# Performance work log

Hardware: AMD Instinct MI355X
Metric: run time of the kernel (lower is better)

The kernel has to match this reference:

```python
import jax, jax.numpy as jnp
import numpy as np
from jax import lax
from jax.scipy.stats import norm

K = 2            # top-k
NUM_EXPERTS = 4
NOISE_EPS = 0.01
LOSS_COEF = 0.01


def conv3x3(x, w):
    # x: [B,Cin,H,W], w: [Cout,Cin,3,3] -> [B,Cout,H,W]
    return lax.conv_general_dilated(x, w, (1, 1), 'SAME',
                                    dimension_numbers=('NCHW', 'OIHW', 'NCHW'))


def setup_inputs() -> dict:
    key = jax.random.key(0)
    ks = jax.random.split(key, 16)
    B, C, H, W = 16, 3, 256, 256
    FC = 2 * C                      # freq channels = 6
    HID = 64
    D = H * W * C                   # flattened gating dim = 196608
    f32 = jnp.float32
    inp = {
        'x':   jax.random.normal(ks[0], (B, C, H, W), f32),
        'ref': jax.random.normal(ks[1], (B, C, H, W), f32),
        'noise': jax.random.normal(ks[2], (B, NUM_EXPERTS), f32),
        'mod_w1': (jax.random.normal(ks[3], (FC, 2 * FC), f32) * 0.1),
        'mod_b1': jnp.zeros((FC,), f32),
        'mod_w2': (jax.random.normal(ks[4], (FC, FC), f32) * 0.1),
        'mod_b2': jnp.zeros((FC,), f32),
        'enh_w': (jax.random.normal(ks[5], (FC, FC), f32) * 0.1),
        'enh_b': jnp.zeros((FC,), f32),
        'fre_prompt': (jax.random.normal(ks[6], (FC, H, W // 2 + 1), f32) * 0.1),
        'w_gate':  (jax.random.normal(ks[7], (D, NUM_EXPERTS), f32) * 0.002),
        'w_noise': (jax.random.normal(ks[8], (D, NUM_EXPERTS), f32) * 0.002),
        'ew1': (jax.random.normal(ks[9],  (NUM_EXPERTS, HID, C, 3, 3), f32) * 0.05),
        'eb1': jnp.zeros((NUM_EXPERTS, HID), f32),
        'ew2': (jax.random.normal(ks[10], (NUM_EXPERTS, 1, HID, 3, 3), f32) * 0.05),
        'eb2': jnp.zeros((NUM_EXPERTS, 1), f32),
    }
    return inp


def _cv_squared(v):
    # torch .var() is unbiased (ddof=1)
    return jnp.var(v, ddof=1) / (jnp.mean(v) ** 2 + 1e-10)


def _forward(x, ref, noise, mod_w1, mod_b1, mod_w2, mod_b2, enh_w, enh_b,
             fre_prompt, w_gate, w_noise, ew1, eb1, ew2, eb2):
    B, C, H, W = x.shape

    # ---- frequency_prompt(ref) ----
    fft = jnp.fft.rfft2(ref, norm='ortho')                    # [B,C,H,W//2+1]
    freq = jnp.concatenate([fft.real, fft.imag], axis=1)      # [B,2C,H,Wf]
    # Adaptive avg/max pool to (H, W//2+1) are identities at native size
    pooled = jnp.concatenate([freq, freq], axis=1)            # [B,4C,H,Wf]
    m = jnp.einsum('oi,bihw->bohw', mod_w1, pooled) + mod_b1[:, None, None]
    m = jax.nn.relu(m)
    m = jnp.einsum('oi,bihw->bohw', mod_w2, m) + mod_b2[:, None, None]
    enh = m * fre_prompt[None]                                # [B,2C,H,Wf]
    enh = jax.nn.relu(jnp.einsum('oi,bihw->bohw', enh_w, enh) + enh_b[:, None, None])
    re, im = jnp.split(enh, 2, axis=1)
    spatial = jnp.fft.irfft2(re + 1j * im, s=(H, W), norm='ortho')  # [B,C,H,W]
    prompt = jax.nn.softmax(spatial.mean(axis=(2, 3), keepdims=True), axis=1)  # [B,C,1,1]

    # ---- noisy top-k gating ----
    x_ds = (x * prompt + x).reshape(B, -1)                    # [B, H*W*C]
    clean_logits = x_ds @ w_gate                              # [B,E]
    noise_stddev = jax.nn.softplus(x_ds @ w_noise) + NOISE_EPS
    noisy_logits = clean_logits + noise * noise_stddev
    top_vals, top_idx = lax.top_k(noisy_logits, K + 1)        # sorted desc, [B,K+1]
    tk_gates = jax.nn.softmax(top_vals[:, :K], axis=1)        # [B,K]
    gates = jnp.zeros_like(noisy_logits).at[
        jnp.arange(B)[:, None], top_idx[:, :K]].set(tk_gates)  # [B,E]

    # load = prob each expert's noisy logit lands in top-k
    thr_in = top_vals[:, K:K + 1]
    thr_out = top_vals[:, K - 1:K]
    is_in = noisy_logits > thr_in
    prob = jnp.where(is_in,
                     norm.cdf((clean_logits - thr_in) / noise_stddev),
                     norm.cdf((clean_logits - thr_out) / noise_stddev))
    load = prob.sum(0)
    importance = gates.sum(0)
    loss = (_cv_squared(importance) + _cv_squared(load)) * LOSS_COEF

    # ---- expert dispatch/combine (== weighted sum; gates are 0 off top-k) ----
    y = jnp.zeros((B, ew2.shape[1], H, W), x.dtype)
    for e in range(NUM_EXPERTS):
        h = jax.nn.relu(conv3x3(x, ew1[e]) + eb1[e][None, :, None, None])
        o = conv3x3(h, ew2[e]) + eb2[e][None, :, None, None]
        y = y + gates[:, e][:, None, None, None] * o
    return y, loss


def reference(x, ref, noise, mod_w1, mod_b1, mod_w2, mod_b2, enh_w, enh_b,
              fre_prompt, w_gate, w_noise, ew1, eb1, ew2, eb2):
    return _forward(x, ref, noise, mod_w1, mod_b1, mod_w2, mod_b2, enh_w, enh_b,
                    fre_prompt, w_gate, w_noise, ew1, eb1, ew2, eb2)
```

## Files before the change

kernel.cpp:

```cpp
#include <hip/hip_runtime.h>
#include <hip/hip_bf16.h>
#include <math.h>

#define WS_GATE 192
#define WS_GNP  256
#define WS_W1F  25088
#define WS_W2F  29184
#define WS_B1P  31616

typedef float    float4v __attribute__((ext_vector_type(4)));
typedef short    short8v __attribute__((ext_vector_type(8)));
typedef _Float16 half8v  __attribute__((ext_vector_type(8)));
typedef _Float16 half2v  __attribute__((ext_vector_type(2)));

union Q4 { uint4 q; short8v s; half8v h; };
union H2 { unsigned u; half2v h; };

__device__ __forceinline__ unsigned short bf16b(float f) {
    unsigned u = __builtin_bit_cast(unsigned, f);
    u = (u + 0x7FFFu + ((u >> 16) & 1u)) >> 16;
    return (unsigned short)u;
}

__device__ __forceinline__ unsigned pkbf16(float a, float b) {
#if __has_builtin(__builtin_amdgcn_cvt_pk_bf16_f32)
    return __builtin_bit_cast(unsigned, __builtin_amdgcn_cvt_pk_bf16_f32(a, b));
#else
    return (unsigned)bf16b(a) | ((unsigned)bf16b(b) << 16);
#endif
}

__device__ __forceinline__ unsigned pkf16(float a, float b) {
#if __has_builtin(__builtin_amdgcn_cvt_pkrtz)
    return __builtin_bit_cast(unsigned, __builtin_amdgcn_cvt_pkrtz(a, b));
#else
    union { _Float16 h[2]; unsigned u; } p;
    p.h[0] = (_Float16)a; p.h[1] = (_Float16)b;
    return p.u;
#endif
}

__device__ __forceinline__ half2v pkmax0(half2v a) {
#if __has_builtin(__builtin_elementwise_max)
    return __builtin_elementwise_max(a, (half2v){(_Float16)0, (_Float16)0});
#else
    half2v r;
    r[0] = a[0] > (_Float16)0 ? a[0] : (_Float16)0;
    r[1] = a[1] > (_Float16)0 ? a[1] : (_Float16)0;
    return r;
#endif
}

__global__ void k_aux(const float* __restrict__ ref, const float* __restrict__ x,
                      const float* __restrict__ wg,  const float* __restrict__ wn,
                      const float* __restrict__ ew1, const float* __restrict__ ew2,
                      const float* __restrict__ eb1,
                      float* __restrict__ ws) {
    __shared__ float sh[4][16][8];
    int blk = blockIdx.x, t = threadIdx.x;

    if (blk < 192) {
        int bc = blk >> 2, chunk = blk & 3;
        const float4* p4 = (const float4*)(ref + (size_t)bc*65536 + (size_t)chunk*16384);
        float acc = 0.f;
        #pragma unroll
        for (int i = 0; i < 16; ++i) { float4 v = p4[i*256 + t]; acc += v.x + v.y + v.z + v.w; }
        #pragma unroll
        for (int m = 1; m <= 32; m <<= 1) acc += __shfl_xor(acc, m);
        if ((t & 63) == 0) sh[0][0][t >> 6] = acc;
        __syncthreads();
        if (t == 0) ws[bc*4 + chunk] = sh[0][0][0] + sh[0][0][1] + sh[0][0][2] + sh[0][0][3];
        return;
    }
    if (blk < 384) {
        int r = blk - 192;
        int c = r >> 6, chunk = r & 63;
        int lane = t & 63, wv = t >> 6;
        int hw0 = chunk*1024 + t*4;
        const float4* wg4 = (const float4*)wg;
        const float4* wn4 = (const float4*)wn;
        const float4* x4  = (const float4*)x;
        float4 G[4], Nw[4];
        #pragma unroll
        for (int i = 0; i < 4; ++i) {
            G[i]  = wg4[c*65536 + hw0 + i];
            Nw[i] = wn4[c*65536 + hw0 + i];
        }
        for (int b = 0; b < 16; ++b) {
            float4 xv = x4[(b*3 + c)*16384 + chunk*256 + t];
            float xs[4] = {xv.x, xv.y, xv.z, xv.w};
            float aG[4] = {0,0,0,0}, aN[4] = {0,0,0,0};
            #pragma unroll
            for (int i = 0; i < 4; ++i) {
                aG[0] += xs[i]*G[i].x;  aG[1] += xs[i]*G[i].y;
                aG[2] += xs[i]*G[i].z;  aG[3] += xs[i]*G[i].w;
                aN[0] += xs[i]*Nw[i].x; aN[1] += xs[i]*Nw[i].y;
                aN[2] += xs[i]*Nw[i].z; aN[3] += xs[i]*Nw[i].w;
            }
            #pragma unroll
            for (int m = 1; m <= 32; m <<= 1) {
                #pragma unroll
                for (int e = 0; e < 4; ++e) {
                    aG[e] += __shfl_xor(aG[e], m);
                    aN[e] += __shfl_xor(aN[e], m);
                }
            }
            if (lane == 0) {
                #pragma unroll
                for (int e = 0; e < 4; ++e) { sh[wv][b][e] = aG[e]; sh[wv][b][4+e] = aN[e]; }
            }
        }
        __syncthreads();
        if (t < 128) {
            int b = t >> 3, s = t & 7;
            float v = sh[0][b][s] + sh[1][b][s] + sh[2][b][s] + sh[3][b][s];
            ws[WS_GNP + ((size_t)(c*64 + chunk)*16 + b)*8 + s] = v;
        }
        return;
    }
    uint4* w1f = (uint4*)(ws + WS_W1F);
    for (int i = t; i < 1024; i += 256) {
        int mm = i & 15, r = i >> 4, qq = r & 3, r2 = r >> 2, f = r2 & 3, e = r2 >> 2;
        const float* w1 = ew1 + e*1728 + (f*16 + mm)*27 + qq*8;
        int navail = 27 - qq*8;
        float v[8];
        #pragma unroll
        for (int j = 0; j < 8; ++j) v[j] = (j < navail) ? w1[j] : 0.f;
        uint4 q;
        q.x = pkbf16(v[0], v[1]); q.y = pkbf16(v[2], v[3]);
        q.z = pkbf16(v[4], v[5]); q.w = pkbf16(v[6], v[7]);
        w1f[i] = q;
    }
    uint4* w2f = (uint4*)(ws + WS_W2F);
    for (int i = t; i < 512; i += 256) {
        int qq = i & 3, r = i >> 2, ks = r & 1, r2 = r >> 1, mm = r2 & 15, e = r2 >> 4;
        uint4 q = make_uint4(0, 0, 0, 0);
        if (mm < 9) {
            float v[8];
            #pragma unroll
            for (int j = 0; j < 8; ++j) v[j] = ew2[e*576 + (ks*32 + qq*8 + j)*9 + mm];
            q.x = pkf16(v[0], v[1]); q.y = pkf16(v[2], v[3]);
            q.z = pkf16(v[4], v[5]); q.w = pkf16(v[6], v[7]);
        }
        w2f[i] = q;
    }
    uint2* b1p = (uint2*)(ws + WS_B1P);
    if (t < 64) {
        int qq = t & 3, r = t >> 2, f = r & 3, e = r >> 2;
        const float* bb = eb1 + e*64 + f*16 + qq*4;
        b1p[t] = make_uint2(pkf16(bb[0], bb[1]), pkf16(bb[2], bb[3]));
    }
}

__global__ void k_gating(const float* __restrict__ noise,
                         const float* __restrict__ mw1, const float* __restrict__ mb1,
                         const float* __restrict__ mw2, const float* __restrict__ mb2,
                         const float* __restrict__ enw, const float* __restrict__ enb,
                         const float* __restrict__ fp,
                         float* __restrict__ ws, float* __restrict__ out) {
    __shared__ float GN2[48*8];
    __shared__ float gL[16][4], pL[16][4], cvs[2];
    int t = threadIdx.x;
    #pragma unroll
    for (int u = 0; u < 3; ++u) {
        int idx = t*3 + u;
        int bc = idx >> 3, s = idx & 7;
        int b = bc / 3, c = bc - b*3;
        float v = 0.f;
        for (int ch = 0; ch < 64; ++ch)
            v += ws[WS_GNP + ((size_t)(c*64 + ch)*16 + b)*8 + s];
        GN2[bc*8 + s] = v;
    }
    __syncthreads();
    if (t < 16) {
        int b = t;
        float sc[3];
        for (int c = 0; c < 3; ++c) {
            int bc = b*3 + c;
            sc[c] = (ws[bc*4] + ws[bc*4+1] + ws[bc*4+2] + ws[bc*4+3]) * (1.f/256.f);
        }
        float pooled[12];
        for (int i = 0; i < 12; ++i) { int r = i % 6; pooled[i] = (r < 3) ? sc[r] : 0.f; }
        float m1[6];
        for (int o = 0; o < 6; ++o) {
            float a = mb1[o];
            for (int i = 0; i < 12; ++i) a += mw1[o*12 + i] * pooled[i];
            m1[o] = fmaxf(a, 0.f);
        }
        float m2[6];
        for (int o = 0; o < 6; ++o) {
            float a = mb2[o];
            for (int i = 0; i < 6; ++i) a += mw2[o*6 + i] * m1[i];
            m2[o] = a * fp[(size_t)o * 33024];
        }
        float dc[3];
        for (int o = 0; o < 3; ++o) {
            float a = enb[o];
            for (int i = 0; i < 6; ++i) a += enw[o*6 + i] * m2[i];
            dc[o] = fmaxf(a, 0.f) * (1.f/256.f);
        }
        float mx = fmaxf(dc[0], fmaxf(dc[1], dc[2]));
        float e0 = expf(dc[0]-mx), e1 = expf(dc[1]-mx), e2 = expf(dc[2]-mx);
        float inv = 1.f / (e0 + e1 + e2);
        float pc[3] = { e0*inv + 1.f, e1*inv + 1.f, e2*inv + 1.f };
        float cl[4], sg[4], nz[4];
        for (int e = 0; e < 4; ++e) {
            float a = 0.f, nr = 0.f;
            for (int c = 0; c < 3; ++c) {
                a  += pc[c] * GN2[(b*3 + c)*8 + e];
                nr += pc[c] * GN2[(b*3 + c)*8 + 4 + e];
            }
            cl[e] = a;
            float sp = (nr > 20.f) ? nr : log1pf(expf(nr));
            sg[e] = sp + 0.01f;
            nz[e] = a + noise[b*4 + e] * sg[e];
        }
        int i0 = 0; float v0 = nz[0];
        for (int e = 1; e < 4; ++e) if (nz[e] > v0) { v0 = nz[e]; i0 = e; }
        int i1 = -1; float v1 = -3.4e38f;
        for (int e = 0; e < 4; ++e) if (e != i0 && nz[e] > v1) { v1 = nz[e]; i1 = e; }
        float v2 = -3.4e38f;
        for (int e = 0; e < 4; ++e) if (e != i0 && e != i1 && nz[e] > v2) v2 = nz[e];
        float ex = expf(v1 - v0), den = 1.f + ex;
        float gate[4] = {0.f, 0.f, 0.f, 0.f};
        gate[i0] = 1.f/den; gate[i1] = ex/den;
        for (int e = 0; e < 4; ++e) {
            ws[WS_GATE + b*4 + e] = gate[e];
            gL[b][e] = gate[e];
            float thr = (nz[e] > v2) ? v2 : v1;
            pL[b][e] = 0.5f * (1.f + erff((cl[e] - thr) / sg[e] * 0.70710678118f));
        }
    }
    __syncthreads();
    if (t < 2) {
        float v[4];
        for (int e = 0; e < 4; ++e) {
            float s = 0.f;
            for (int b = 0; b < 16; ++b) s += (t == 0) ? gL[b][e] : pL[b][e];
            v[e] = s;
        }
        float mean = 0.25f * (v[0] + v[1] + v[2] + v[3]);
        float var = 0.f;
        for (int e = 0; e < 4; ++e) { float d = v[e] - mean; var += d*d; }
        var *= (1.f/3.f);
        cvs[t] = var / (mean*mean + 1e-10f);
    }
    __syncthreads();
    if (t == 0) out[1048576] = (cvs[0] + cvs[1]) * 0.01f;
}

__global__ __launch_bounds__(256, 3)
void k_experts(const float* __restrict__ x, const float* __restrict__ eb2,
               const float* __restrict__ ws, float* __restrict__ out) {
    __shared__ __align__(16) uint4 s_hid[324*8];
    __shared__ __align__(16) char  s_mix[11808];
    float* in_s = (float*)s_mix;
    float* s_T  = (float*)s_mix;

    int t = threadIdx.x;
    int bid = blockIdx.x;
    int logical = (bid & 7) * 512 + (bid >> 3);
    int b = logical >> 8, tile = logical & 255;
    int ty0 = (tile >> 4) * 16, tx0 = (tile & 15) * 16;
    const float* xb = x + (size_t)b * 196608;

    for (int i = t; i < 1200; i += 256) {
        int ci = i / 400, r = i - ci*400, iy = r / 20, ix = r - iy*20;
        int gy = ty0 - 2 + iy, gx = tx0 - 2 + ix;
        float v = 0.f;
        if ((unsigned)gy < 256u && (unsigned)gx < 256u) v = xb[ci*65536 + gy*256 + gx];
        in_s[i] = v;
    }
    __syncthreads();

    int lane = t & 63, wv = t >> 6;
    int qq = lane >> 4, mm = lane & 15;
    int oy = t >> 4, ox = t & 15;

    int offj[8];
    #pragma unroll
    for (int j = 0; j < 8; ++j) {
        int k = qq*8 + j;
        if (k < 27) { int ci = k/9, r = k - ci*9, kh = r/3, kw = r - kh*3;
                      offj[j] = ci*400 + kh*20 + kw; }
        else offj[j] = -1;
    }

    Q4 bfr[6];
    #pragma unroll
    for (int i = 0; i < 6; ++i) {
        int gidx = wv + i*4;
        if (gidx >= 21) break;
        int p = gidx*16 + mm;
        int py = p/18, px = p - py*18;
        int base = (p < 324) ? (py*20 + px) : 0;
        float v[8];
        #pragma unroll
        for (int j = 0; j < 8; ++j)
            v[j] = (offj[j] >= 0) ? in_s[base + offj[j]] : 0.f;
        bfr[i].q.x = pkbf16(v[0], v[1]); bfr[i].q.y = pkbf16(v[2], v[3]);
        bfr[i].q.z = pkbf16(v[4], v[5]); bfr[i].q.w = pkbf16(v[6], v[7]);
    }

    bool interior = (ty0 > 0) && (ty0 < 240) && (tx0 > 0) && (tx0 < 240);
    const float4 gates = *(const float4*)(ws + WS_GATE + b*4);
    float gv[4] = {gates.x, gates.y, gates.z, gates.w};
    const uint4* w1f = (const uint4*)(ws + WS_W1F);
    const uint4* w2f = (const uint4*)(ws + WS_W2F);
    const uint2* b1p = (const uint2*)(ws + WS_B1P);
    float accY = 0.f;

    for (int e = 0; e < 4; ++e) {
        float g = gv[e];
        if (g == 0.f) continue;

        Q4 bw0, bw1;
        bw0.q = w2f[((e*16 + mm)*2 + 0)*4 + qq];
        bw1.q = w2f[((e*16 + mm)*2 + 1)*4 + qq];

        Q4 af[4];
        H2 bias01[4], bias23[4];
        #pragma unroll
        for (int f = 0; f < 4; ++f) {
            af[f].q = w1f[((e*4 + f)*4 + qq)*16 + mm];
            uint2 bp = b1p[(e*4 + f)*4 + qq];
            bias01[f].u = bp.x; bias23[f].u = bp.y;
        }

        #pragma unroll
        for (int i = 0; i < 6; ++i) {
            int gidx = wv + i*4;
            if (gidx >= 21) break;
            int p = gidx*16 + mm;
            bool valid = p < 324;
            H2 mskv;
            if (!interior) {
                int py = p/18, px = p - py*18;
                int gy = ty0 - 1 + py, gx = tx0 - 1 + px;
                float msk = (((unsigned)gy < 256u) && ((unsigned)gx < 256u)) ? 1.f : 0.f;
                mskv.u = pkf16(msk, msk);
            }
            #pragma unroll
            for (int f = 0; f < 4; ++f) {
                float4v d = __builtin_amdgcn_mfma_f32_16x16x32_bf16(
                    af[f].s, bfr[i].s, (float4v){0.f,0.f,0.f,0.f}, 0, 0, 0);
                if (valid) {
                    H2 h01, h23;
                    h01.u = pkf16(d[0], d[1]);
                    h23.u = pkf16(d[2], d[3]);
                    h01.h = pkmax0(h01.h + bias01[f].h);
                    h23.h = pkmax0(h23.h + bias23[f].h);
                    if (!interior) { h01.h = h01.h * mskv.h; h23.h = h23.h * mskv.h; }
                    uint2 pk = make_uint2(h01.u, h23.u);
                    int ch0 = f*16 + qq*4;
                    int hchunk = ch0 >> 3, hsel = (ch0 >> 2) & 1;
                    ((uint2*)&s_hid[p*8 + ((hchunk + p) & 7)])[hsel] = pk;
                }
            }
        }
        __syncthreads();

        for (int gi = wv; gi < 21; gi += 4) {
            int base = gi*16; if (base > 308) base = 308;
            int p = base + mm;
            Q4 a0, a1;
            a0.q = s_hid[p*8 + ((qq + p) & 7)];
            a1.q = s_hid[p*8 + ((4 + qq + p) & 7)];
            float4v d = __builtin_amdgcn_mfma_f32_16x16x32_f16(
                a0.h, bw0.h, (float4v){0.f,0.f,0.f,0.f}, 0, 0, 0);
            d = __builtin_amdgcn_mfma_f32_16x16x32_f16(a1.h, bw1.h, d, 0, 0, 0);
            if (mm < 9) {
                float4* dst = (float4*)&s_T[mm*328 + base + qq*4];
                *dst = make_float4(d[0], d[1], d[2], d[3]);
            }
        }
        __syncthreads();

        float oacc = 0.f;
        #pragma unroll
        for (int kh = 0; kh < 3; ++kh) {
            #pragma unroll
            for (int kw = 0; kw < 3; ++kw)
                oacc += s_T[(kh*3 + kw)*328 + (oy + kh)*18 + ox + kw];
        }
        accY += g * (oacc + eb2[e]);
    }
    out[(size_t)b*65536 + (ty0 + oy)*256 + tx0 + ox] = accY;
}

extern "C" void kernel_launch(void* const* d_in, const int* in_sizes, int n_in,
                              void* d_out, int out_size, void* d_ws, size_t ws_size,
                              hipStream_t stream) {
    (void)in_sizes; (void)n_in; (void)out_size; (void)ws_size;
    const float* x     = (const float*)d_in[0];
    const float* ref   = (const float*)d_in[1];
    const float* noise = (const float*)d_in[2];
    const float* mw1   = (const float*)d_in[3];
    const float* mb1   = (const float*)d_in[4];
    const float* mw2   = (const float*)d_in[5];
    const float* mb2   = (const float*)d_in[6];
    const float* enw   = (const float*)d_in[7];
    const float* enb   = (const float*)d_in[8];
    const float* fp    = (const float*)d_in[9];
    const float* wg    = (const float*)d_in[10];
    const float* wn    = (const float*)d_in[11];
    const float* ew1   = (const float*)d_in[12];
    const float* eb1   = (const float*)d_in[13];
    const float* ew2   = (const float*)d_in[14];
    const float* eb2   = (const float*)d_in[15];
    float* out = (float*)d_out;
    float* ws  = (float*)d_ws;

    k_aux    <<<385, 256, 0, stream>>>(ref, x, wg, wn, ew1, ew2, eb1, ws);
    k_gating <<<1, 128, 0, stream>>>(noise, mw1, mb1, mw2, mb2, enw, enb, fp, ws, out);
    k_experts<<<4096, 256, 0, stream>>>(x, eb2, ws, out);
}
```

Before: 182.6 us.

## Split expert tile per wave to drop block barriers; atomically reduce gating partials

Each wave of the expert kernel now owns four output rows and their 6x18 halo of hidden pixels (7 groups of 16). The hidden activations go through a small per-wave LDS exchange buffer and per-wave s_T scratch, so lgkmcnt waits replace the two block-wide __syncthreads per expert. Each wave now recomputes overlapping halo rows (7 groups per wave instead of about 5.25), which adds MFMA work in exchange for removing the barriers and shrinking LDS so occupancy can rise to 4 blocks. The gating partial sums are accumulated with atomicAdd into a buffer zeroed by a memset, replacing the 64-way loop in the single-block gating kernel, at the cost of one extra memset launch.

```diff
diff --git a/kernel.cpp b/kernel.cpp
--- a/kernel.cpp
+++ b/kernel.cpp
@@ -49,6 +49,10 @@
     r[1] = a[1] > (_Float16)0 ? a[1] : (_Float16)0;
     return r;
 #endif
+}
+
+__device__ __forceinline__ void wave_fence() {
+    asm volatile("s_waitcnt lgkmcnt(0)" ::: "memory");
 }
 
 __global__ void k_aux(const float* __restrict__ ref, const float* __restrict__ x,
@@ -114,7 +118,7 @@
         if (t < 128) {
             int b = t >> 3, s = t & 7;
             float v = sh[0][b][s] + sh[1][b][s] + sh[2][b][s] + sh[3][b][s];
-            ws[WS_GNP + ((size_t)(c*64 + chunk)*16 + b)*8 + s] = v;
+            atomicAdd(&ws[WS_GNP + (b*3 + c)*8 + s], v);
         }
         return;
     }
@@ -164,12 +168,7 @@
     #pragma unroll
     for (int u = 0; u < 3; ++u) {
         int idx = t*3 + u;
-        int bc = idx >> 3, s = idx & 7;
-        int b = bc / 3, c = bc - b*3;
-        float v = 0.f;
-        for (int ch = 0; ch < 64; ++ch)
-            v += ws[WS_GNP + ((size_t)(c*64 + ch)*16 + b)*8 + s];
-        GN2[bc*8 + s] = v;
+        GN2[idx] = ws[WS_GNP + idx];
     }
     __syncthreads();
     if (t < 16) {
@@ -249,13 +248,12 @@
     if (t == 0) out[1048576] = (cvs[0] + cvs[1]) * 0.01f;
 }
 
-__global__ __launch_bounds__(256, 3)
+__global__ __launch_bounds__(256, 4)
 void k_experts(const float* __restrict__ x, const float* __restrict__ eb2,
                const float* __restrict__ ws, float* __restrict__ out) {
-    __shared__ __align__(16) uint4 s_hid[324*8];
-    __shared__ __align__(16) char  s_mix[11808];
-    float* in_s = (float*)s_mix;
-    float* s_T  = (float*)s_mix;
+    __shared__ __align__(16) float in_s[1200];
+    __shared__ __align__(16) uint4 s_exch[4][16][9];
+    __shared__ __align__(16) float s_T[4][9][116];
 
     int t = threadIdx.x;
     int bid = blockIdx.x;
@@ -275,7 +273,6 @@
 
     int lane = t & 63, wv = t >> 6;
     int qq = lane >> 4, mm = lane & 15;
-    int oy = t >> 4, ox = t & 15;
 
     int offj[8];
     #pragma unroll
@@ -286,106 +283,91 @@
         else offj[j] = -1;
     }
 
-    Q4 bfr[6];
+    bool interior = (ty0 > 0) && (ty0 < 240) && (tx0 > 0) && (tx0 < 240);
+
+    Q4 bfr[7];
+    H2 mskg[7];
     #pragma unroll
-    for (int i = 0; i < 6; ++i) {
-        int gidx = wv + i*4;
-        if (gidx >= 21) break;
-        int p = gidx*16 + mm;
+    for (int grp = 0; grp < 7; ++grp) {
+        int p = wv*72 + grp*16 + mm;
         int py = p/18, px = p - py*18;
         int base = (p < 324) ? (py*20 + px) : 0;
         float v[8];
         #pragma unroll
         for (int j = 0; j < 8; ++j)
             v[j] = (offj[j] >= 0) ? in_s[base + offj[j]] : 0.f;
-        bfr[i].q.x = pkbf16(v[0], v[1]); bfr[i].q.y = pkbf16(v[2], v[3]);
-        bfr[i].q.z = pkbf16(v[4], v[5]); bfr[i].q.w = pkbf16(v[6], v[7]);
-    }
-
-    bool interior = (ty0 > 0) && (ty0 < 240) && (tx0 > 0) && (tx0 < 240);
+        bfr[grp].q.x = pkbf16(v[0], v[1]); bfr[grp].q.y = pkbf16(v[2], v[3]);
+        bfr[grp].q.z = pkbf16(v[4], v[5]); bfr[grp].q.w = pkbf16(v[6], v[7]);
+        if (!interior) {
+            int gy = ty0 - 1 + py, gx = tx0 - 1 + px;
+            float msk = (((unsigned)gy < 256u) && ((unsigned)gx < 256u)) ? 1.f : 0.f;
+            mskg[grp].u = pkf16(msk, msk);
+        }
+    }
+
     const float4 gates = *(const float4*)(ws + WS_GATE + b*4);
     float gv[4] = {gates.x, gates.y, gates.z, gates.w};
     const uint4* w1f = (const uint4*)(ws + WS_W1F);
     const uint4* w2f = (const uint4*)(ws + WS_W2F);
     const uint2* b1p = (const uint2*)(ws + WS_B1P);
+
+    uint2* exw = (uint2*)&s_exch[wv][mm][0];
+    const uint4* exr = &s_exch[wv][mm][0];
     float accY = 0.f;
 
     for (int e = 0; e < 4; ++e) {
-        float g = gv[e];
-        if (g == 0.f) continue;
+        float gval = gv[e];
+        if (gval == 0.f) continue;
 
         Q4 bw0, bw1;
         bw0.q = w2f[((e*16 + mm)*2 + 0)*4 + qq];
         bw1.q = w2f[((e*16 + mm)*2 + 1)*4 + qq];
-
-        Q4 af[4];
-        H2 bias01[4], bias23[4];
+        Q4 af[4]; H2 b01[4], b23[4];
         #pragma unroll
         for (int f = 0; f < 4; ++f) {
             af[f].q = w1f[((e*4 + f)*4 + qq)*16 + mm];
             uint2 bp = b1p[(e*4 + f)*4 + qq];
-            bias01[f].u = bp.x; bias23[f].u = bp.y;
-        }
-
-        #pragma unroll
-        for (int i = 0; i < 6; ++i) {
-            int gidx = wv + i*4;
-            if (gidx >= 21) break;
-            int p = gidx*16 + mm;
-            bool valid = p < 324;
-            H2 mskv;
-            if (!interior) {
-                int py = p/18, px = p - py*18;
-                int gy = ty0 - 1 + py, gx = tx0 - 1 + px;
-                float msk = (((unsigned)gy < 256u) && ((unsigned)gx < 256u)) ? 1.f : 0.f;
-                mskv.u = pkf16(msk, msk);
-            }
+            b01[f].u = bp.x; b23[f].u = bp.y;
+        }
+
+        #pragma unroll
+        for (int grp = 0; grp < 7; ++grp) {
             #pragma unroll
             for (int f = 0; f < 4; ++f) {
                 float4v d = __builtin_amdgcn_mfma_f32_16x16x32_bf16(
-                    af[f].s, bfr[i].s, (float4v){0.f,0.f,0.f,0.f}, 0, 0, 0);
-                if (valid) {
-                    H2 h01, h23;
-                    h01.u = pkf16(d[0], d[1]);
-                    h23.u = pkf16(d[2], d[3]);
-                    h01.h = pkmax0(h01.h + bias01[f].h);
-                    h23.h = pkmax0(h23.h + bias23[f].h);
-                    if (!interior) { h01.h = h01.h * mskv.h; h23.h = h23.h * mskv.h; }
-                    uint2 pk = make_uint2(h01.u, h23.u);
-                    int ch0 = f*16 + qq*4;
-                    int hchunk = ch0 >> 3, hsel = (ch0 >> 2) & 1;
-                    ((uint2*)&s_hid[p*8 + ((hchunk + p) & 7)])[hsel] = pk;
-                }
+                    af[f].s, bfr[grp].s, (float4v){0.f,0.f,0.f,0.f}, 0, 0, 0);
+                H2 h01, h23;
+                h01.u = pkf16(d[0], d[1]);
+                h23.u = pkf16(d[2], d[3]);
+                h01.h = pkmax0(h01.h + b01[f].h);
+                h23.h = pkmax0(h23.h + b23[f].h);
+                if (!interior) { h01.h = h01.h * mskg[grp].h; h23.h = h23.h * mskg[grp].h; }
+                exw[f*4 + qq] = make_uint2(h01.u, h23.u);
             }
-        }
-        __syncthreads();
-
-        for (int gi = wv; gi < 21; gi += 4) {
-            int base = gi*16; if (base > 308) base = 308;
-            int p = base + mm;
+            wave_fence();
+
             Q4 a0, a1;
-            a0.q = s_hid[p*8 + ((qq + p) & 7)];
-            a1.q = s_hid[p*8 + ((4 + qq + p) & 7)];
-            float4v d = __builtin_amdgcn_mfma_f32_16x16x32_f16(
+            a0.q = exr[qq];
+            a1.q = exr[4 + qq];
+            float4v d2 = __builtin_amdgcn_mfma_f32_16x16x32_f16(
                 a0.h, bw0.h, (float4v){0.f,0.f,0.f,0.f}, 0, 0, 0);
-            d = __builtin_amdgcn_mfma_f32_16x16x32_f16(a1.h, bw1.h, d, 0, 0, 0);
-            if (mm < 9) {
-                float4* dst = (float4*)&s_T[mm*328 + base + qq*4];
-                *dst = make_float4(d[0], d[1], d[2], d[3]);
-            }
-        }
-        __syncthreads();
+            d2 = __builtin_amdgcn_mfma_f32_16x16x32_f16(a1.h, bw1.h, d2, 0, 0, 0);
+            if (mm < 9)
+                *(float4*)&s_T[wv][mm][grp*16 + qq*4] = make_float4(d2[0], d2[1], d2[2], d2[3]);
+            wave_fence();
+        }
 
         float oacc = 0.f;
         #pragma unroll
         for (int kh = 0; kh < 3; ++kh) {
             #pragma unroll
             for (int kw = 0; kw < 3; ++kw)
-                oacc += s_T[(kh*3 + kw)*328 + (oy + kh)*18 + ox + kw];
-        }
-        accY += g * (oacc + eb2[e]);
-    }
-    out[(size_t)b*65536 + (ty0 + oy)*256 + tx0 + ox] = accY;
+                oacc += s_T[wv][kh*3 + kw][(qq + kh)*18 + mm + kw];
+        }
+        wave_fence();
+        accY += gval * (oacc + eb2[e]);
+    }
+    out[(size_t)b*65536 + (ty0 + wv*4 + qq)*256 + tx0 + mm] = accY;
 }
 
 extern "C" void kernel_launch(void* const* d_in, const int* in_sizes, int n_in,
@@ -411,6 +393,7 @@
     float* out = (float*)d_out;
     float* ws  = (float*)d_ws;
 
+    hipMemsetAsync(ws + WS_GNP, 0, 384*sizeof(float), stream);
     k_aux    <<<385, 256, 0, stream>>>(ref, x, wg, wn, ew1, ew2, eb1, ws);
     k_gating <<<1, 128, 0, stream>>>(noise, mw1, mb1, mw2, mb2, enw, enb, fp, ws, out);
     k_experts<<<4096, 256, 0, stream>>>(x, eb2, ws, out);
```

Result: faster. 172.8 us (-5.4%).
